# Performance work log

Measured on AMD Instinct MI355X. Metric: run time of the kernel, lower is better.

The kernel has to match this reference:

```python
import jax, jax.numpy as jnp
import numpy as np

HEADS = 16


def _linear(x, w, b):
    # torch nn.Linear: y = x @ W^T + b, W: (out, in)
    return jnp.einsum('bld,od->blo', x, w) + b


def setup_inputs() -> dict:
    key = jax.random.key(0)
    ks = jax.random.split(key, 11)
    B, L, QD, KVD = 8, 2048, 1024, 1024
    s_in = 1.0 / np.sqrt(QD)
    return {
        'query': jax.random.normal(ks[0], (B, L, QD), jnp.float32),
        'key':   jax.random.normal(ks[1], (B, L, KVD), jnp.float32),
        'value': jax.random.normal(ks[2], (B, L, KVD), jnp.float32),
        'wq_w': jax.random.normal(ks[3], (KVD, QD), jnp.float32) * s_in,
        'wq_b': jnp.zeros((KVD,), jnp.float32),
        'wk_w': jax.random.normal(ks[4], (KVD, KVD), jnp.float32) * s_in,
        'wk_b': jnp.zeros((KVD,), jnp.float32),
        'wv_w': jax.random.normal(ks[5], (KVD, KVD), jnp.float32) * s_in,
        'wv_b': jnp.zeros((KVD,), jnp.float32),
        'fo_w': jax.random.normal(ks[6], (QD, KVD), jnp.float32) * s_in,
        'fo_b': jnp.zeros((QD,), jnp.float32),
    }


def reference(query, key, value, wq_w, wq_b, wk_w, wk_b, wv_w, wv_b, fo_w, fo_b):
    B, Lq, _ = query.shape
    Lk = key.shape[1]
    kvd = wq_w.shape[0]
    head_dim = kvd // HEADS
    # reshape WITHOUT transpose, exactly as the torch source: (B, L, heads, head_dim)
    q = _linear(query, wq_w, wq_b).reshape(B, Lq, HEADS, head_dim)
    k = _linear(key,   wk_w, wk_b).reshape(B, Lk, HEADS, head_dim)
    v = _linear(value, wv_w, wv_b).reshape(B, Lk, HEADS, head_dim)
    scale = 1.0 / jnp.sqrt(jnp.float32(head_dim))
    # Faithful to source: seq axis acts as 'h'; heads axis is contracted (i,j).
    scores = jnp.einsum('bhid,bhjd->bhij', q, k) * scale  # (B, L, heads, heads)
    weights = jax.nn.softmax(scores, axis=-1)
    out = jnp.einsum('bhij,bhjd->bhid', weights, v)       # (B, L, heads, head_dim)
    out = out.reshape(B, Lq, kvd)
    return _linear(out, fo_w, fo_b)
```

## Files before the change

kernel.cpp:

```cpp
#include <hip/hip_runtime.h>
#include <hip/hip_bf16.h>


typedef __attribute__((ext_vector_type(8))) __bf16 bf16x8;
typedef __attribute__((ext_vector_type(4))) float f32x4;

#define BM 128
#define BN 128
#define BK 64

__device__ __forceinline__ float bf2f(ushort u) {
  union { unsigned int i; float f; } c; c.i = ((unsigned int)u) << 16; return c.f;
}
__device__ __forceinline__ ushort f2b(float f) {
  union { float f; unsigned int i; } c; c.f = f;
  unsigned int x = c.i;
  return (ushort)((x + 0x7FFFu + ((x >> 16) & 1u)) >> 16);
}

__global__ __launch_bounds__(256)
void cvt_f32_bf16(const float* __restrict__ s, ushort* __restrict__ d, int n8)
{
  int i = blockIdx.x * 256 + threadIdx.x;
  if (i >= n8) return;
  const float4* sp = reinterpret_cast<const float4*>(s) + (size_t)i * 2;
  float4 a = sp[0], b = sp[1];
  ushort u[8] = { f2b(a.x), f2b(a.y), f2b(a.z), f2b(a.w),
                  f2b(b.x), f2b(b.y), f2b(b.z), f2b(b.w) };
  reinterpret_cast<uint4*>(d)[i] = *reinterpret_cast<uint4*>(u);
}

__global__ __launch_bounds__(256)
void cvt_in3(const float* __restrict__ a, const float* __restrict__ b,
             const float* __restrict__ c, ushort* __restrict__ dst, int n8each)
{
  int i = blockIdx.x * 256 + threadIdx.x;
  if (i >= 3 * n8each) return;
  const float* s; int j;
  if (i < n8each)          { s = a; j = i; }
  else if (i < 2 * n8each) { s = b; j = i - n8each; }
  else                     { s = c; j = i - 2 * n8each; }
  const float4* sp = reinterpret_cast<const float4*>(s) + (size_t)j * 2;
  float4 x = sp[0], y = sp[1];
  ushort u[8] = { f2b(x.x), f2b(x.y), f2b(x.z), f2b(x.w),
                  f2b(y.x), f2b(y.y), f2b(y.z), f2b(y.w) };
  reinterpret_cast<uint4*>(dst)[i] = *reinterpret_cast<uint4*>(u);
}

__global__ __launch_bounds__(256)
void cvt_wo_perm(const float* __restrict__ w, ushort* __restrict__ o)
{
  int t = blockIdx.x * 256 + threadIdx.x;
  int n  = t >> 7;
  int i8 = (t & 127) << 3;
  int blk = i8 >> 8, g = (i8 >> 6) & 3, c = (i8 >> 2) & 15;
  const float* src = w + (size_t)n * 1024 + 4 * g * 64 + blk * 16 + c;
  ushort u[8];
  #pragma unroll
  for (int j = 0; j < 8; ++j)
    u[j] = f2b(src[(j & 3) * 64 + (j >> 2)]);
  *reinterpret_cast<uint4*>(o + (size_t)n * 1024 + i8) = *reinterpret_cast<uint4*>(u);
}

template<int CMODE>
__device__ __forceinline__
void gemm_body(const ushort* __restrict__ A, const ushort* __restrict__ Bw,
               const float* __restrict__ bias, void* __restrict__ Cv,
               int N, int K, ushort* lds)
{
  const int tid  = threadIdx.x;
  const int lane = tid & 63;
  const int wid  = tid >> 6;
  const int wm   = wid >> 2;
  const int wn   = wid & 3;

  const int nwg = gridDim.x * gridDim.y;
  int fid = blockIdx.y * gridDim.x + blockIdx.x;
  if ((nwg & 7) == 0) fid = (fid & 7) * (nwg >> 3) + (fid >> 3);
  const int bx = fid % gridDim.x;
  const int by = fid / gridDim.x;
  const int m0 = by * 256, n0 = bx * 256;

  const int NT = K >> 6;

  const int csw = ((lane & 7) ^ (lane >> 3)) << 3;
  auto STAGE = [&](int h, int kt) {
    const ushort* base = (h >= 2) ? Bw : A;
    const int o0 = (h >= 2) ? n0 : m0;
    const int rl = (h & 1) * 128;
    #pragma unroll
    for (int j = 0; j < 2; ++j) {
      int rt = rl + j * 64 + wid * 8;
      const ushort* src = base + (size_t)(o0 + rt + (lane >> 3)) * K + kt * 64 + csw;
      ushort* dst = lds + (h >= 2 ? 16384 : 0) + rt * 64;
      __builtin_amdgcn_global_load_lds(
          (const __attribute__((address_space(1))) void*)src,
          (__attribute__((address_space(3))) void*)dst, 16, 0, 0);
    }
  };

  auto LDA = [&](int mi, int kk) -> bf16x8 {
    int row  = (mi & 3) * 16 + wm * 64 + (mi >> 2) * 128 + (lane & 15);
    int slot = kk * 4 + (lane >> 4);
    int byte = row * 128 + (((slot ^ (row & 7)) & 7) << 4);
    return *reinterpret_cast<const bf16x8*>((const char*)lds + byte);
  };
  auto LDB = [&](int ni, int kk) -> bf16x8 {
    int row  = (ni & 1) * 16 + wn * 32 + (ni >> 1) * 128 + (lane & 15);
    int slot = kk * 4 + (lane >> 4);
    int byte = row * 128 + (((slot ^ (row & 7)) & 7) << 4);
    return *reinterpret_cast<const bf16x8*>((const char*)(lds + 16384) + byte);
  };

  f32x4 acc[8][4] = {};
  bf16x8 af[4][2], bf[4][2];

  STAGE(0, 0); STAGE(2, 0); STAGE(3, 0); STAGE(1, 0);
  asm volatile("s_waitcnt vmcnt(4)" ::: "memory");
  __builtin_amdgcn_s_barrier();

  for (int t = 0; t < NT; ++t) {
    const bool pf = (t + 1) < NT;

    #pragma unroll
    for (int i = 0; i < 4; ++i) { af[i][0] = LDA(i, 0); af[i][1] = LDA(i, 1); }
    #pragma unroll
    for (int n = 0; n < 2; ++n) { bf[n][0] = LDB(n, 0); bf[n][1] = LDB(n, 1); }
    asm volatile("s_waitcnt vmcnt(2)" ::: "memory");
    __builtin_amdgcn_s_barrier();
    __builtin_amdgcn_s_setprio(1);
    #pragma unroll
    for (int i = 0; i < 4; ++i)
      #pragma unroll
      for (int n = 0; n < 2; ++n)
        #pragma unroll
        for (int kk = 0; kk < 2; ++kk)
          acc[i][n] = __builtin_amdgcn_mfma_f32_16x16x32_bf16(af[i][kk], bf[n][kk], acc[i][n], 0, 0, 0);
    __builtin_amdgcn_s_setprio(0);
    asm volatile("s_waitcnt lgkmcnt(0)" ::: "memory");
    __builtin_amdgcn_s_barrier();

    if (pf) { STAGE(0, t + 1); STAGE(2, t + 1); }
    #pragma unroll
    for (int n = 0; n < 2; ++n) { bf[2 + n][0] = LDB(2 + n, 0); bf[2 + n][1] = LDB(2 + n, 1); }
    if (pf) asm volatile("s_waitcnt vmcnt(4)" ::: "memory");
    else    asm volatile("s_waitcnt vmcnt(0)" ::: "memory");
    __builtin_amdgcn_s_barrier();
    __builtin_amdgcn_s_setprio(1);
    #pragma unroll
    for (int i = 0; i < 4; ++i)
      #pragma unroll
      for (int n = 0; n < 2; ++n)
        #pragma unroll
        for (int kk = 0; kk < 2; ++kk)
          acc[i][2 + n] = __builtin_amdgcn_mfma_f32_16x16x32_bf16(af[i][kk], bf[2 + n][kk], acc[i][2 + n], 0, 0, 0);
    __builtin_amdgcn_s_setprio(0);
    asm volatile("s_waitcnt lgkmcnt(0)" ::: "memory");
    __builtin_amdgcn_s_barrier();

    if (pf) STAGE(3, t + 1);
    #pragma unroll
    for (int i = 0; i < 4; ++i) { af[i][0] = LDA(4 + i, 0); af[i][1] = LDA(4 + i, 1); }
    __builtin_amdgcn_s_barrier();
    __builtin_amdgcn_s_setprio(1);
    #pragma unroll
    for (int i = 0; i < 4; ++i)
      #pragma unroll
      for (int n = 0; n < 2; ++n)
        #pragma unroll
        for (int kk = 0; kk < 2; ++kk)
          acc[4 + i][n] = __builtin_amdgcn_mfma_f32_16x16x32_bf16(af[i][kk], bf[n][kk], acc[4 + i][n], 0, 0, 0);
    __builtin_amdgcn_s_setprio(0);
    asm volatile("s_waitcnt lgkmcnt(0)" ::: "memory");
    __builtin_amdgcn_s_barrier();

    if (pf) { STAGE(1, t + 1);
              asm volatile("s_waitcnt vmcnt(4)" ::: "memory"); }
    __builtin_amdgcn_s_barrier();
    __builtin_amdgcn_s_setprio(1);
    #pragma unroll
    for (int i = 0; i < 4; ++i)
      #pragma unroll
      for (int n = 0; n < 2; ++n)
        #pragma unroll
        for (int kk = 0; kk < 2; ++kk)
          acc[4 + i][2 + n] = __builtin_amdgcn_mfma_f32_16x16x32_bf16(af[i][kk], bf[2 + n][kk], acc[4 + i][2 + n], 0, 0, 0);
    __builtin_amdgcn_s_setprio(0);
    __builtin_amdgcn_s_barrier();
  }

  #pragma unroll
  for (int ni = 0; ni < 4; ++ni) {
    int col = n0 + (ni & 1) * 16 + wn * 32 + (ni >> 1) * 128 + (lane & 15);
    float bv = bias[col];
    #pragma unroll
    for (int mi = 0; mi < 8; ++mi) {
      int row0 = m0 + (mi & 3) * 16 + wm * 64 + (mi >> 2) * 128 + ((lane >> 4) << 2);
      #pragma unroll
      for (int q = 0; q < 4; ++q) {
        float v = acc[mi][ni][q] + bv;
        if constexpr (CMODE == 0)
          ((float*)Cv)[(size_t)(row0 + q) * N + col] = v;
        else
          ((ushort*)Cv)[(size_t)(row0 + q) * N + col] = f2b(v);
      }
    }
  }
}

template<int CMODE>
__global__ __launch_bounds__(512, 2)
void gemm8p(const ushort* __restrict__ A, const ushort* __restrict__ Bw,
            const float* __restrict__ bias, void* __restrict__ Cv,
            int M, int N, int K)
{
  extern __shared__ ushort lds[];
  gemm_body<CMODE>(A, Bw, bias, Cv, N, K, lds);
}

__global__ __launch_bounds__(512, 2)
void gemm8p_qkv(const ushort* __restrict__ Abase, const ushort* __restrict__ Wbase,
                const float* __restrict__ b0, const float* __restrict__ b1,
                const float* __restrict__ b2, ushort* __restrict__ Cbase,
                int M, int N, int K)
{
  extern __shared__ ushort lds[];
  const int z = blockIdx.z;
  const size_t slot = (size_t)M * K;
  const size_t wsl  = (size_t)N * K;
  const float* bias = (z == 0) ? b0 : (z == 1) ? b1 : b2;
  gemm_body<1>(Abase + z * slot, Wbase + z * wsl, bias,
               (void*)(Cbase + z * (size_t)M * N), N, K, lds);
}

__global__ __launch_bounds__(256)
void attn_mfma2(const ushort* __restrict__ Q, const ushort* __restrict__ Kh,
                const ushort* __restrict__ V, ushort* __restrict__ Ot, int P)
{
  const int lane = threadIdx.x & 63;
  const int wid  = threadIdx.x >> 6;
  const int g = lane >> 4, c = lane & 15;
  const int stride = gridDim.x * 4;

  for (int p = blockIdx.x * 4 + wid; p < P; p += stride) {
    const ushort* qb = Q  + (size_t)p * 1024;
    const ushort* kb = Kh + (size_t)p * 1024;
    const ushort* vb = V  + (size_t)p * 1024;

    bf16x8 qf0 = *reinterpret_cast<const bf16x8*>(qb + c * 64 + g * 8);
    bf16x8 qf1 = *reinterpret_cast<const bf16x8*>(qb + c * 64 + 32 + g * 8);
    bf16x8 kf0 = *reinterpret_cast<const bf16x8*>(kb + c * 64 + g * 8);
    bf16x8 kf1 = *reinterpret_cast<const bf16x8*>(kb + c * 64 + 32 + g * 8);

    f32x4 s = {};
    s = __builtin_amdgcn_mfma_f32_16x16x32_bf16(kf0, qf0, s, 0, 0, 0);
    s = __builtin_amdgcn_mfma_f32_16x16x32_bf16(kf1, qf1, s, 0, 0, 0);

    float s0 = s[0] * 0.125f, s1 = s[1] * 0.125f;
    float s2 = s[2] * 0.125f, s3 = s[3] * 0.125f;
    float m = fmaxf(fmaxf(s0, s1), fmaxf(s2, s3));
    m = fmaxf(m, __shfl_xor(m, 16));
    m = fmaxf(m, __shfl_xor(m, 32));
    float e0 = __expf(s0 - m), e1 = __expf(s1 - m);
    float e2 = __expf(s2 - m), e3 = __expf(s3 - m);
    float sum = e0 + e1 + e2 + e3;
    sum += __shfl_xor(sum, 16);
    sum += __shfl_xor(sum, 32);
    float r = 1.0f / sum;

    uint pk0 = (uint)f2b(e0 * r) | ((uint)f2b(e1 * r) << 16);
    uint pk1 = (uint)f2b(e2 * r) | ((uint)f2b(e3 * r) << 16);

    int srcA = (((2 * g) & 3) << 4) | c;
    int srcB = (((2 * g + 1) & 3) << 4) | c;
    uint a0 = (uint)__shfl((int)pk0, srcA);
    uint a1 = (uint)__shfl((int)pk1, srcA);
    uint a2 = (uint)__shfl((int)pk0, srcB);
    uint a3 = (uint)__shfl((int)pk1, srcB);
    if (g >= 2) { a0 = 0; a1 = 0; a2 = 0; a3 = 0; }
    union { uint u[4]; bf16x8 v; } pa;
    pa.u[0] = a0; pa.u[1] = a1; pa.u[2] = a2; pa.u[3] = a3;

    ushort* ob = Ot + (size_t)p * 1024;
    #pragma unroll
    for (int blk = 0; blk < 4; ++blk) {
      union { ushort u[8]; bf16x8 v; } vf;
      #pragma unroll
      for (int e = 0; e < 8; ++e)
        vf.u[e] = vb[(8 * (g & 1) + e) * 64 + blk * 16 + c];
      f32x4 o = {};
      o = __builtin_amdgcn_mfma_f32_16x16x32_bf16(pa.v, vf.v, o, 0, 0, 0);
      uint lo = (uint)f2b(o[0]) | ((uint)f2b(o[1]) << 16);
      uint hi = (uint)f2b(o[2]) | ((uint)f2b(o[3]) << 16);
      uint2 w2; w2.x = lo; w2.y = hi;
      *reinterpret_cast<uint2*>(ob + blk * 256 + g * 64 + c * 4) = w2;
    }
  }
}

template<bool A_IS_BF16, bool OUT_BF16>
__global__ __launch_bounds__(256)
void gemm_bt(const void* __restrict__ Av, const float* __restrict__ B,
             const float* __restrict__ bias, void* __restrict__ Cv,
             int M, int N, int K)
{
  __shared__ ushort As[BM * BK];
  __shared__ ushort Bs[BN * BK];

  const int tid  = threadIdx.x;
  const int lane = tid & 63;
  const int wid  = tid >> 6;
  const int wr   = wid >> 1;
  const int wc   = wid & 1;
  const int m0   = blockIdx.y * BM;
  const int n0   = blockIdx.x * BN;

  f32x4 acc[4][4] = {};

  const int r   = tid >> 1;
  const int seg = (tid & 1) * 32;

  for (int k0 = 0; k0 < K; k0 += BK) {
    {
      ushort tmp[32];
      if constexpr (A_IS_BF16) {
        const ushort* gA = (const ushort*)Av + (size_t)(m0 + r) * K + k0 + seg;
        #pragma unroll
        for (int u = 0; u < 4; ++u)
          *reinterpret_cast<uint4*>(&tmp[u * 8]) =
              *reinterpret_cast<const uint4*>(gA + u * 8);
      } else {
        const float* gA = (const float*)Av + (size_t)(m0 + r) * K + k0 + seg;
        #pragma unroll
        for (int u = 0; u < 8; ++u) {
          float4 f = *reinterpret_cast<const float4*>(gA + u * 4);
          tmp[u * 4 + 0] = f2b(f.x); tmp[u * 4 + 1] = f2b(f.y);
          tmp[u * 4 + 2] = f2b(f.z); tmp[u * 4 + 3] = f2b(f.w);
        }
      }
      #pragma unroll
      for (int s4 = 0; s4 < 4; ++s4) {
        int slot = (seg >> 3) + s4;
        int byte = r * 128 + ((slot ^ (r & 7)) << 4);
        *reinterpret_cast<uint4*>((char*)As + byte) =
            *reinterpret_cast<uint4*>(&tmp[s4 * 8]);
      }
    }
    {
      const float* gB = B + (size_t)(n0 + r) * K + k0 + seg;
      ushort tmp[32];
      #pragma unroll
      for (int u = 0; u < 8; ++u) {
        float4 f = *reinterpret_cast<const float4*>(gB + u * 4);
        tmp[u * 4 + 0] = f2b(f.x); tmp[u * 4 + 1] = f2b(f.y);
        tmp[u * 4 + 2] = f2b(f.z); tmp[u * 4 + 3] = f2b(f.w);
      }
      #pragma unroll
      for (int s4 = 0; s4 < 4; ++s4) {
        int slot = (seg >> 3) + s4;
        int byte = r * 128 + ((slot ^ (r & 7)) << 4);
        *reinterpret_cast<uint4*>((char*)Bs + byte) =
            *reinterpret_cast<uint4*>(&tmp[s4 * 8]);
      }
    }
    __syncthreads();

    #pragma unroll
    for (int kk = 0; kk < 2; ++kk) {
      const int kbase = kk * 32 + ((lane >> 4) << 3);
      const int slot  = kbase >> 3;
      bf16x8 af[4], bfr[4];
      #pragma unroll
      for (int mi = 0; mi < 4; ++mi) {
        int row = wr * 64 + mi * 16 + (lane & 15);
        af[mi] = *reinterpret_cast<const bf16x8*>(
            (const char*)As + row * 128 + ((slot ^ (row & 7)) << 4));
      }
      #pragma unroll
      for (int ni = 0; ni < 4; ++ni) {
        int row = wc * 64 + ni * 16 + (lane & 15);
        bfr[ni] = *reinterpret_cast<const bf16x8*>(
            (const char*)Bs + row * 128 + ((slot ^ (row & 7)) << 4));
      }
      #pragma unroll
      for (int mi = 0; mi < 4; ++mi)
        #pragma unroll
        for (int ni = 0; ni < 4; ++ni)
          acc[mi][ni] = __builtin_amdgcn_mfma_f32_16x16x32_bf16(
              af[mi], bfr[ni], acc[mi][ni], 0, 0, 0);
    }
    __syncthreads();
  }

  #pragma unroll
  for (int ni = 0; ni < 4; ++ni) {
    int col = n0 + wc * 64 + ni * 16 + (lane & 15);
    float bv = bias[col];
    #pragma unroll
    for (int mi = 0; mi < 4; ++mi) {
      int row0 = m0 + wr * 64 + mi * 16 + ((lane >> 4) << 2);
      #pragma unroll
      for (int q = 0; q < 4; ++q) {
        float v = acc[mi][ni][q] + bv;
        if constexpr (OUT_BF16)
          ((ushort*)Cv)[(size_t)(row0 + q) * N + col] = f2b(v);
        else
          ((float*)Cv)[(size_t)(row0 + q) * N + col] = v;
      }
    }
  }
}

__global__ __launch_bounds__(256)
void attn_kernel(const ushort* __restrict__ Q, const ushort* __restrict__ Kh,
                 const ushort* __restrict__ V, ushort* __restrict__ O)
{
  __shared__ float smem[4][3][16][68];
  const int tid  = threadIdx.x;
  const int wid  = tid >> 6;
  const int lane = tid & 63;
  const size_t p = (size_t)blockIdx.x * 4 + wid;

  {
    const ushort* srcs[3] = { Q + p * 1024, Kh + p * 1024, V + p * 1024 };
    const int i  = lane >> 2;
    const int d0 = (lane & 3) * 16;
    #pragma unroll
    for (int m = 0; m < 3; ++m) {
      const ushort* s = srcs[m] + lane * 16;
      ushort u[16];
      *reinterpret_cast<uint4*>(&u[0]) = *reinterpret_cast<const uint4*>(s);
      *reinterpret_cast<uint4*>(&u[8]) = *reinterpret_cast<const uint4*>(s + 8);
      #pragma unroll
      for (int e = 0; e < 16; ++e) smem[wid][m][i][d0 + e] = bf2f(u[e]);
    }
  }
  __syncthreads();

  const int i  = lane >> 2;
  const int jg = lane & 3;
  const float* qrow = smem[wid][0][i];
  const float* k0r = smem[wid][1][jg * 4 + 0];
  const float* k1r = smem[wid][1][jg * 4 + 1];
  const float* k2r = smem[wid][1][jg * 4 + 2];
  const float* k3r = smem[wid][1][jg * 4 + 3];

  float s0 = 0.f, s1 = 0.f, s2 = 0.f, s3 = 0.f;
  #pragma unroll
  for (int d = 0; d < 64; ++d) {
    float qv = qrow[d];
    s0 += qv * k0r[d]; s1 += qv * k1r[d];
    s2 += qv * k2r[d]; s3 += qv * k3r[d];
  }
  const float scale = 0.125f;
  s0 *= scale; s1 *= scale; s2 *= scale; s3 *= scale;

  float mx = fmaxf(fmaxf(s0, s1), fmaxf(s2, s3));
  mx = fmaxf(mx, __shfl_xor(mx, 1));
  mx = fmaxf(mx, __shfl_xor(mx, 2));
  float e0 = __expf(s0 - mx), e1 = __expf(s1 - mx);
  float e2 = __expf(s2 - mx), e3 = __expf(s3 - mx);
  float sum = e0 + e1 + e2 + e3;
  sum += __shfl_xor(sum, 1);
  sum += __shfl_xor(sum, 2);
  float inv = 1.0f / sum;
  e0 *= inv; e1 *= inv; e2 *= inv; e3 *= inv;

  const float* v0r = smem[wid][2][jg * 4 + 0];
  const float* v1r = smem[wid][2][jg * 4 + 1];
  const float* v2r = smem[wid][2][jg * 4 + 2];
  const float* v3r = smem[wid][2][jg * 4 + 3];
  ushort* orow = O + p * 1024 + i * 64;

  #pragma unroll
  for (int cc = 0; cc < 4; ++cc) {
    float po[16];
    #pragma unroll
    for (int dd = 0; dd < 16; ++dd) {
      int d = cc * 16 + dd;
      po[dd] = e0 * v0r[d] + e1 * v1r[d] + e2 * v2r[d] + e3 * v3r[d];
    }
    #pragma unroll
    for (int dd = 0; dd < 16; ++dd) {
      po[dd] += __shfl_xor(po[dd], 1);
      po[dd] += __shfl_xor(po[dd], 2);
    }
    if (jg == cc) {
      #pragma unroll
      for (int dd = 0; dd < 16; ++dd) orow[cc * 16 + dd] = f2b(po[dd]);
    }
  }
}

extern "C" void kernel_launch(void* const* d_in, const int* in_sizes, int n_in,
                              void* d_out, int out_size, void* d_ws, size_t ws_size,
                              hipStream_t stream)
{
  const float* query = (const float*)d_in[0];
  const float* key_  = (const float*)d_in[1];
  const float* value = (const float*)d_in[2];
  const float* wq_w  = (const float*)d_in[3];
  const float* wq_b  = (const float*)d_in[4];
  const float* wk_w  = (const float*)d_in[5];
  const float* wk_b  = (const float*)d_in[6];
  const float* wv_w  = (const float*)d_in[7];
  const float* wv_b  = (const float*)d_in[8];
  const float* fo_w  = (const float*)d_in[9];
  const float* fo_b  = (const float*)d_in[10];

  const int K = 1024, N = 1024;
  const int M = in_sizes[0] / K;
  const size_t slot = (size_t)M * N;
  const size_t wsl  = (size_t)N * K;
  const size_t need_big = (6 * slot + 4 * wsl) * sizeof(ushort);
  const size_t need_mid = (4 * slot + 4 * wsl) * sizeof(ushort);
  const bool dims_ok = (M % 256) == 0 && N == 1024 && K == 1024;

  const int n8w = (int)(wsl / 8);
  const int n8s = (int)(slot / 8);

  if (ws_size >= need_big && dims_ok) {
    hipFuncSetAttribute(reinterpret_cast<const void*>(gemm8p<0>),
                        hipFuncAttributeMaxDynamicSharedMemorySize, 65536);
    hipFuncSetAttribute(reinterpret_cast<const void*>(gemm8p_qkv),
                        hipFuncAttributeMaxDynamicSharedMemorySize, 65536);

    ushort* I0 = (ushort*)d_ws;
    ushort* P1 = I0 + 3 * slot;
    ushort* Wq = P1 + 3 * slot;
    ushort* Wo = Wq + 3 * wsl;
    ushort* Ot = I0;

    dim3 g8(N / 256, M / 256);
    dim3 g8z(N / 256, M / 256, 3);
    dim3 b8(512);

    cvt_in3<<<dim3((3 * n8s + 255) / 256), dim3(256), 0, stream>>>(
        query, key_, value, I0, n8s);
    cvt_in3<<<dim3((3 * n8w + 255) / 256), dim3(256), 0, stream>>>(
        wq_w, wk_w, wv_w, Wq, n8w);
    cvt_wo_perm<<<dim3(512), dim3(256), 0, stream>>>(fo_w, Wo);

    gemm8p_qkv<<<g8z, b8, 65536, stream>>>(I0, Wq, wq_b, wk_b, wv_b, P1, M, N, K);

    attn_mfma2<<<dim3(2048), dim3(256), 0, stream>>>(
        P1, P1 + slot, P1 + 2 * slot, Ot, M);
    gemm8p<0><<<g8, b8, 65536, stream>>>(Ot, Wo, fo_b, d_out, M, N, K);
  } else if (ws_size >= need_mid && dims_ok) {
    hipFuncSetAttribute(reinterpret_cast<const void*>(gemm8p<0>),
                        hipFuncAttributeMaxDynamicSharedMemorySize, 65536);
    hipFuncSetAttribute(reinterpret_cast<const void*>(gemm8p<1>),
                        hipFuncAttributeMaxDynamicSharedMemorySize, 65536);

    ushort* S0 = (ushort*)d_ws;
    ushort* S1 = S0 + slot;
    ushort* S2 = S1 + slot;
    ushort* S3 = S2 + slot;
    ushort* Wq = S3 + slot;
    ushort* Wo = Wq + 3 * wsl;

    dim3 g8(N / 256, M / 256);
    dim3 b8(512);

    cvt_in3<<<dim3((3 * n8w + 255) / 256), dim3(256), 0, stream>>>(
        wq_w, wk_w, wv_w, Wq, n8w);
    cvt_wo_perm<<<dim3(512), dim3(256), 0, stream>>>(fo_w, Wo);

    cvt_f32_bf16<<<dim3((n8s + 255) / 256), dim3(256), 0, stream>>>(query, S0, n8s);
    gemm8p<1><<<g8, b8, 65536, stream>>>(S0, Wq,           wq_b, S1, M, N, K);
    cvt_f32_bf16<<<dim3((n8s + 255) / 256), dim3(256), 0, stream>>>(key_, S0, n8s);
    gemm8p<1><<<g8, b8, 65536, stream>>>(S0, Wq + wsl,     wk_b, S2, M, N, K);
    cvt_f32_bf16<<<dim3((n8s + 255) / 256), dim3(256), 0, stream>>>(value, S0, n8s);
    gemm8p<1><<<g8, b8, 65536, stream>>>(S0, Wq + 2 * wsl, wv_b, S3, M, N, K);

    attn_mfma2<<<dim3(2048), dim3(256), 0, stream>>>(S1, S2, S3, S0, M);
    gemm8p<0><<<g8, b8, 65536, stream>>>(S0, Wo, fo_b, d_out, M, N, K);
  } else {
    dim3 grid(N / BN, M / BM);
    ushort* Qb = (ushort*)d_ws;
    ushort* Kb = Qb + slot;
    ushort* Vb = Kb + slot;
    ushort* Ob = Vb + slot;
    gemm_bt<false, true><<<grid, dim3(256), 0, stream>>>(query, wq_w, wq_b, Qb, M, N, K);
    gemm_bt<false, true><<<grid, dim3(256), 0, stream>>>(key_,  wk_w, wk_b, Kb, M, N, K);
    gemm_bt<false, true><<<grid, dim3(256), 0, stream>>>(value, wv_w, wv_b, Vb, M, N, K);
    attn_kernel<<<dim3(M / 4), dim3(256), 0, stream>>>(Qb, Kb, Vb, Ob);
    gemm_bt<true, false><<<grid, dim3(256), 0, stream>>>(Ob, fo_w, fo_b, d_out, M, N, K);
  }
}
```

Measured before the change: 229.5 us.

## Switch GEMM core to 32x32x16 MFMA with MFMA-native LDS tile layout

Replaces the 16x16x32 bf16 MFMA inner product with the 32x32x16 variant and reorganizes the LDS staging layout so each 32-row group is stored contiguously in the fragment order the MFMA reads, dropping the XOR swizzle. Accumulators become f32x16 per 32x32 tile and the epilogue is rewritten to match the new output lane mapping. The larger MFMA shape is meant to cut LDS fragment reads and instruction count per FLOP. The occupancy hint of 2 blocks per CU is removed from launch bounds. The new LDS layout may introduce bank conflicts, and the 32-lane column stores in the epilogue are less coalesced.

```diff
diff --git a/kernel.cpp b/kernel.cpp
--- a/kernel.cpp
+++ b/kernel.cpp
@@ -4,6 +4,7 @@
 
 typedef __attribute__((ext_vector_type(8))) __bf16 bf16x8;
 typedef __attribute__((ext_vector_type(4))) float f32x4;
+typedef __attribute__((ext_vector_type(16))) float f32x16;
 
 #define BM 128
 #define BN 128
@@ -83,37 +84,35 @@
 
   const int NT = K >> 6;
 
-  const int csw = ((lane & 7) ^ (lane >> 3)) << 3;
   auto STAGE = [&](int h, int kt) {
     const ushort* base = (h >= 2) ? Bw : A;
     const int o0 = (h >= 2) ? n0 : m0;
-    const int rl = (h & 1) * 128;
+    const int hh = h & 1;
     #pragma unroll
     for (int j = 0; j < 2; ++j) {
-      int rt = rl + j * 64 + wid * 8;
-      const ushort* src = base + (size_t)(o0 + rt + (lane >> 3)) * K + kt * 64 + csw;
-      ushort* dst = lds + (h >= 2 ? 16384 : 0) + rt * 64;
+      int cI = wid * 2 + j;
+      int rt = hh * 4 + (cI >> 2);
+      int g0 = (cI & 3) * 2;
+      const ushort* src = base + (size_t)(o0 + rt * 32 + (lane & 31)) * K
+                          + kt * 64 + (g0 + (lane >> 5)) * 8;
+      ushort* dst = lds + (h >= 2 ? 16384 : 0) + rt * 2048 + g0 * 256;
       __builtin_amdgcn_global_load_lds(
           (const __attribute__((address_space(1))) void*)src,
           (__attribute__((address_space(3))) void*)dst, 16, 0, 0);
     }
   };
 
-  auto LDA = [&](int mi, int kk) -> bf16x8 {
-    int row  = (mi & 3) * 16 + wm * 64 + (mi >> 2) * 128 + (lane & 15);
-    int slot = kk * 4 + (lane >> 4);
-    int byte = row * 128 + (((slot ^ (row & 7)) & 7) << 4);
+  auto LDA = [&](int tg, int ks) -> bf16x8 {
+    int byte = tg * 4096 + (ks * 2 + (lane >> 5)) * 512 + (lane & 31) * 16;
     return *reinterpret_cast<const bf16x8*>((const char*)lds + byte);
   };
-  auto LDB = [&](int ni, int kk) -> bf16x8 {
-    int row  = (ni & 1) * 16 + wn * 32 + (ni >> 1) * 128 + (lane & 15);
-    int slot = kk * 4 + (lane >> 4);
-    int byte = row * 128 + (((slot ^ (row & 7)) & 7) << 4);
+  auto LDB = [&](int tg, int ks) -> bf16x8 {
+    int byte = tg * 4096 + (ks * 2 + (lane >> 5)) * 512 + (lane & 31) * 16;
     return *reinterpret_cast<const bf16x8*>((const char*)(lds + 16384) + byte);
   };
 
-  f32x4 acc[8][4] = {};
-  bf16x8 af[4][2], bf[4][2];
+  f32x16 acc[4][2] = {};
+  bf16x8 afr[2][4], bflo[4], bfhi[4];
 
   STAGE(0, 0); STAGE(2, 0); STAGE(3, 0); STAGE(1, 0);
   asm volatile("s_waitcnt vmcnt(4)" ::: "memory");
@@ -123,53 +122,51 @@
     const bool pf = (t + 1) < NT;
 
     #pragma unroll
-    for (int i = 0; i < 4; ++i) { af[i][0] = LDA(i, 0); af[i][1] = LDA(i, 1); }
-    #pragma unroll
-    for (int n = 0; n < 2; ++n) { bf[n][0] = LDB(n, 0); bf[n][1] = LDB(n, 1); }
+    for (int r = 0; r < 2; ++r)
+      #pragma unroll
+      for (int ks = 0; ks < 4; ++ks) afr[r][ks] = LDA(wm * 2 + r, ks);
+    #pragma unroll
+    for (int ks = 0; ks < 4; ++ks) bflo[ks] = LDB(wn, ks);
     asm volatile("s_waitcnt vmcnt(2)" ::: "memory");
     __builtin_amdgcn_s_barrier();
     __builtin_amdgcn_s_setprio(1);
     #pragma unroll
-    for (int i = 0; i < 4; ++i)
-      #pragma unroll
-      for (int n = 0; n < 2; ++n)
-        #pragma unroll
-        for (int kk = 0; kk < 2; ++kk)
-          acc[i][n] = __builtin_amdgcn_mfma_f32_16x16x32_bf16(af[i][kk], bf[n][kk], acc[i][n], 0, 0, 0);
+    for (int ks = 0; ks < 4; ++ks)
+      #pragma unroll
+      for (int r = 0; r < 2; ++r)
+        acc[r][0] = __builtin_amdgcn_mfma_f32_32x32x16_bf16(afr[r][ks], bflo[ks], acc[r][0], 0, 0, 0);
     __builtin_amdgcn_s_setprio(0);
     asm volatile("s_waitcnt lgkmcnt(0)" ::: "memory");
     __builtin_amdgcn_s_barrier();
 
     if (pf) { STAGE(0, t + 1); STAGE(2, t + 1); }
     #pragma unroll
-    for (int n = 0; n < 2; ++n) { bf[2 + n][0] = LDB(2 + n, 0); bf[2 + n][1] = LDB(2 + n, 1); }
+    for (int ks = 0; ks < 4; ++ks) bfhi[ks] = LDB(wn + 4, ks);
     if (pf) asm volatile("s_waitcnt vmcnt(4)" ::: "memory");
     else    asm volatile("s_waitcnt vmcnt(0)" ::: "memory");
     __builtin_amdgcn_s_barrier();
     __builtin_amdgcn_s_setprio(1);
     #pragma unroll
-    for (int i = 0; i < 4; ++i)
-      #pragma unroll
-      for (int n = 0; n < 2; ++n)
-        #pragma unroll
-        for (int kk = 0; kk < 2; ++kk)
-          acc[i][2 + n] = __builtin_amdgcn_mfma_f32_16x16x32_bf16(af[i][kk], bf[2 + n][kk], acc[i][2 + n], 0, 0, 0);
+    for (int ks = 0; ks < 4; ++ks)
+      #pragma unroll
+      for (int r = 0; r < 2; ++r)
+        acc[r][1] = __builtin_amdgcn_mfma_f32_32x32x16_bf16(afr[r][ks], bfhi[ks], acc[r][1], 0, 0, 0);
     __builtin_amdgcn_s_setprio(0);
     asm volatile("s_waitcnt lgkmcnt(0)" ::: "memory");
     __builtin_amdgcn_s_barrier();
 
     if (pf) STAGE(3, t + 1);
     #pragma unroll
-    for (int i = 0; i < 4; ++i) { af[i][0] = LDA(4 + i, 0); af[i][1] = LDA(4 + i, 1); }
+    for (int r = 0; r < 2; ++r)
+      #pragma unroll
+      for (int ks = 0; ks < 4; ++ks) afr[r][ks] = LDA(wm * 2 + 4 + r, ks);
     __builtin_amdgcn_s_barrier();
     __builtin_amdgcn_s_setprio(1);
     #pragma unroll
-    for (int i = 0; i < 4; ++i)
-      #pragma unroll
-      for (int n = 0; n < 2; ++n)
-        #pragma unroll
-        for (int kk = 0; kk < 2; ++kk)
-          acc[4 + i][n] = __builtin_amdgcn_mfma_f32_16x16x32_bf16(af[i][kk], bf[n][kk], acc[4 + i][n], 0, 0, 0);
+    for (int ks = 0; ks < 4; ++ks)
+      #pragma unroll
+      for (int r = 0; r < 2; ++r)
+        acc[2 + r][0] = __builtin_amdgcn_mfma_f32_32x32x16_bf16(afr[r][ks], bflo[ks], acc[2 + r][0], 0, 0, 0);
     __builtin_amdgcn_s_setprio(0);
     asm volatile("s_waitcnt lgkmcnt(0)" ::: "memory");
     __builtin_amdgcn_s_barrier();
@@ -179,37 +176,36 @@
     __builtin_amdgcn_s_barrier();
     __builtin_amdgcn_s_setprio(1);
     #pragma unroll
-    for (int i = 0; i < 4; ++i)
-      #pragma unroll
-      for (int n = 0; n < 2; ++n)
-        #pragma unroll
-        for (int kk = 0; kk < 2; ++kk)
-          acc[4 + i][2 + n] = __builtin_amdgcn_mfma_f32_16x16x32_bf16(af[i][kk], bf[2 + n][kk], acc[4 + i][2 + n], 0, 0, 0);
+    for (int ks = 0; ks < 4; ++ks)
+      #pragma unroll
+      for (int r = 0; r < 2; ++r)
+        acc[2 + r][1] = __builtin_amdgcn_mfma_f32_32x32x16_bf16(afr[r][ks], bfhi[ks], acc[2 + r][1], 0, 0, 0);
     __builtin_amdgcn_s_setprio(0);
     __builtin_amdgcn_s_barrier();
   }
 
   #pragma unroll
-  for (int ni = 0; ni < 4; ++ni) {
-    int col = n0 + (ni & 1) * 16 + wn * 32 + (ni >> 1) * 128 + (lane & 15);
+  for (int c = 0; c < 2; ++c) {
+    int col = n0 + wn * 32 + c * 128 + (lane & 31);
     float bv = bias[col];
     #pragma unroll
-    for (int mi = 0; mi < 8; ++mi) {
-      int row0 = m0 + (mi & 3) * 16 + wm * 64 + (mi >> 2) * 128 + ((lane >> 4) << 2);
-      #pragma unroll
-      for (int q = 0; q < 4; ++q) {
-        float v = acc[mi][ni][q] + bv;
+    for (int r = 0; r < 4; ++r) {
+      int row0 = m0 + (r & 1) * 32 + wm * 64 + (r >> 1) * 128 + 4 * (lane >> 5);
+      #pragma unroll
+      for (int g = 0; g < 16; ++g) {
+        int row = row0 + (g & 3) + 8 * (g >> 2);
+        float v = acc[r][c][g] + bv;
         if constexpr (CMODE == 0)
-          ((float*)Cv)[(size_t)(row0 + q) * N + col] = v;
+          ((float*)Cv)[(size_t)row * N + col] = v;
         else
-          ((ushort*)Cv)[(size_t)(row0 + q) * N + col] = f2b(v);
+          ((ushort*)Cv)[(size_t)row * N + col] = f2b(v);
       }
     }
   }
 }
 
 template<int CMODE>
-__global__ __launch_bounds__(512, 2)
+__global__ __launch_bounds__(512)
 void gemm8p(const ushort* __restrict__ A, const ushort* __restrict__ Bw,
             const float* __restrict__ bias, void* __restrict__ Cv,
             int M, int N, int K)
@@ -218,7 +214,7 @@
   gemm_body<CMODE>(A, Bw, bias, Cv, N, K, lds);
 }
 
-__global__ __launch_bounds__(512, 2)
+__global__ __launch_bounds__(512)
 void gemm8p_qkv(const ushort* __restrict__ Abase, const ushort* __restrict__ Wbase,
                 const float* __restrict__ b0, const float* __restrict__ b1,
                 const float* __restrict__ b2, ushort* __restrict__ Cbase,
```

Result: slower. 242.9 us (+5.8%).
